# Kernel optimization log

Measured on AMD Instinct MI355X. Metric: run time of the kernel, lower is better.

The kernel has to match this reference:

```python
import jax, jax.numpy as jnp
import numpy as np

LN_EPS = 1e-5


def setup_inputs() -> dict:
    key = jax.random.key(0)
    ks = jax.random.split(key, 10)
    N, E, B = 20000, 320000, 16
    node_dim, cond_dim, out_dim = 256, 512, 256
    return {
        "node_feats": jax.random.normal(ks[0], (N, node_dim), dtype=jnp.float32),
        "cond_feats": jax.random.normal(ks[1], (B, cond_dim), dtype=jnp.float32),
        "batch_ids": jax.random.randint(ks[2], (N,), 0, B),
        "node_j_ids": jax.random.randint(ks[3], (E,), 0, N),
        "node_i_ids": jax.random.randint(ks[4], (E,), 0, N),
        "edge_w": jax.random.uniform(ks[5], (E, 1), dtype=jnp.float32),
        "edge_p": jax.random.uniform(ks[6], (E, 1), dtype=jnp.float32),
        "Wc": jax.random.normal(ks[7], (cond_dim, 2 * out_dim), dtype=jnp.float32) * (cond_dim ** -0.5),
        "bc": jax.random.normal(ks[8], (2 * out_dim,), dtype=jnp.float32) * 0.02,
        "Wl": jax.random.normal(ks[9], (node_dim, out_dim), dtype=jnp.float32) * (node_dim ** -0.5),
    }


def reference(node_feats, cond_feats, batch_ids, node_j_ids, node_i_ids,
              edge_w, edge_p, Wc, bc, Wl):
    N = node_feats.shape[0]
    # --- FiLM fusion ---
    gb = cond_feats @ Wc + bc                       # [B, 2*out_dim]
    gamma, beta = jnp.split(gb, 2, axis=-1)
    gamma = gamma + 1.0
    x = node_feats @ Wl                             # [N, out_dim]
    # non-affine LayerNorm over last dim
    mu = jnp.mean(x, axis=-1, keepdims=True)
    var = jnp.mean(jnp.square(x - mu), axis=-1, keepdims=True)
    x = (x - mu) * jax.lax.rsqrt(var + LN_EPS)
    x = x * gamma[batch_ids] + beta[batch_ids]      # per-node FiLM via batch gather
    x = jax.nn.relu(x)
    # --- message passing: gather -> weight -> scatter-add ---
    edge_weights = edge_w * edge_p                  # [E, 1]
    msg = x[node_j_ids] * edge_weights              # [E, out_dim]
    agg = jax.ops.segment_sum(msg, node_i_ids, num_segments=N)
    return jax.nn.relu(agg)
```

## Files before the change

### kernel.cpp

```cpp
#include <hip/hip_runtime.h>
#include <hip/hip_bf16.h>

#define OUT_DIM 256
#define COND_DIM 512
#define NODE_DIM 256
#define TM 32
#define LDA 264
#define LN_EPS 1e-5f
#define CAP 64
#define POISON 0xAAAAAAAAu
#define CHUNK 4096
#define EPT 16
#define NBINS 256
#define BCAP 2560

typedef __attribute__((ext_vector_type(8))) short bf16x8;
typedef __attribute__((ext_vector_type(8))) unsigned short u16x8;
typedef __attribute__((ext_vector_type(4))) float f32x4;

__device__ inline unsigned short f2bf(float f) {
    unsigned u = __float_as_uint(f);
    u += 0x7fffu + ((u >> 16) & 1u);
    return (unsigned short)(u >> 16);
}
__device__ inline float bf2f(unsigned short b) {
    return __uint_as_float((unsigned)b << 16);
}

__global__ __launch_bounds__(256) void f1_prep_kernel(
        const int* __restrict__ ni, const int* __restrict__ nj,
        const float* __restrict__ ew, const float* __restrict__ ep,
        unsigned* __restrict__ gcur, unsigned* __restrict__ coarse_ij,
        float* __restrict__ coarse_w, int E, int f1b,
        const float* __restrict__ Wl, unsigned short* __restrict__ WlT,
        const float* __restrict__ cond, const float* __restrict__ Wc,
        const float* __restrict__ bc, float* __restrict__ gamma, float* __restrict__ beta) {
    __shared__ float lds[64 * 65];
    __shared__ unsigned cnt[NBINS], base[NBINS];
    int t = threadIdx.x;

    if (blockIdx.x < (unsigned)f1b) {
        cnt[t] = 0;
        __syncthreads();
        unsigned ijr[EPT]; float wr[EPT]; unsigned rbr[EPT];
        int e0 = blockIdx.x * CHUNK;
        #pragma unroll
        for (int k = 0; k < EPT; ++k) {
            int e = e0 + k * 256 + t;
            if (e < E) {
                unsigned i = (unsigned)ni[e];
                unsigned j = (unsigned)nj[e];
                float w = ew[e] * ep[e];
                unsigned b = i >> 7;
                unsigned r = atomicAdd(&cnt[b], 1u);
                ijr[k] = (i << 16) | j;
                wr[k]  = w;
                rbr[k] = r | (b << 20);
            } else rbr[k] = 0xFFFFFFFFu;
        }
        __syncthreads();
        {
            unsigned c = cnt[t];
            base[t] = c ? (atomicAdd(&gcur[t], c) - POISON) : 0u;
        }
        __syncthreads();
        #pragma unroll
        for (int k = 0; k < EPT; ++k) {
            if (rbr[k] != 0xFFFFFFFFu) {
                unsigned b = rbr[k] >> 20;
                unsigned pos = base[b] + (rbr[k] & 0xFFFFFu);
                if (pos < BCAP) {
                    unsigned idx = b * BCAP + pos;
                    coarse_ij[idx] = ijr[k];
                    coarse_w[idx]  = wr[k];
                }
            }
        }
        return;
    }

    int pb = blockIdx.x - f1b;
    if (pb < 16) {
        float (*tile)[65] = (float(*)[65])lds;
        int bx = pb & 3, by = pb >> 2;
        int tr = t >> 6, tc = t & 63;
        #pragma unroll
        for (int rr = 0; rr < 64; rr += 4)
            tile[rr + tr][tc] = Wl[(by * 64 + rr + tr) * OUT_DIM + bx * 64 + tc];
        __syncthreads();
        #pragma unroll
        for (int rr = 0; rr < 64; rr += 4) {
            int n = bx * 64 + rr + tr;
            int k = by * 64 + tc;
            WlT[n * NODE_DIM + k] = f2bf(tile[tc][rr + tr]);
        }
    } else {
        int bf = pb - 16;
        int b = bf >> 1, half = bf & 1;
        int o = half * 256 + t;
        float* c = lds;
        for (int k = t; k < COND_DIM; k += 256) c[k] = cond[b * COND_DIM + k];
        __syncthreads();
        float acc = bc[o];
        for (int k = 0; k < COND_DIM; k += 4) {
            float4 cv = *(const float4*)&c[k];
            acc += cv.x * Wc[(k + 0) * 512 + o];
            acc += cv.y * Wc[(k + 1) * 512 + o];
            acc += cv.z * Wc[(k + 2) * 512 + o];
            acc += cv.w * Wc[(k + 3) * 512 + o];
        }
        if (half == 0) gamma[b * 256 + t] = acc + 1.0f;
        else           beta[b * 256 + t] = acc;
    }
}

__global__ __launch_bounds__(256) void f2_gemm_kernel(
        const unsigned* __restrict__ gcur, const unsigned* __restrict__ coarse_ij,
        const float* __restrict__ coarse_w, unsigned* __restrict__ epk,
        unsigned* __restrict__ cursor, int NB,
        const float* __restrict__ nf, const unsigned short* __restrict__ WlT,
        const int* __restrict__ batch_ids, const float* __restrict__ gamma,
        const float* __restrict__ beta, unsigned short* __restrict__ xout, int N) {
    __shared__ __align__(16) unsigned short Atile[TM * LDA];
    __shared__ float part_s[TM][2], part_s2[TM][2];
    __shared__ int bid_s[TM];
    __shared__ unsigned lcur[128];
    int t = threadIdx.x;

    if (blockIdx.x < (unsigned)NB) {
        int b = blockIdx.x;
        if (t < 128) lcur[t] = 0;
        __syncthreads();
        unsigned cntb = gcur[b] - POISON;
        if (cntb > BCAP) cntb = BCAP;
        for (unsigned r = t; r < cntb; r += 256) {
            unsigned ij = coarse_ij[(unsigned)b * BCAP + r];
            float w = coarse_w[(unsigned)b * BCAP + r];
            unsigned i = ij >> 16;
            unsigned c = atomicAdd(&lcur[i & 127u], 1u);
            if (c < CAP)
                epk[(i << 6) + c] = (ij & 0xFFFFu) | ((unsigned)f2bf(w) << 16);
        }
        __syncthreads();
        if (t < 128) cursor[(unsigned)b * 128 + t] = lcur[t];
        return;
    }

    int n0 = (blockIdx.x - NB) * TM;

    #pragma unroll
    for (int it = 0; it < 8; ++it) {
        int idx = t + it * 256;
        int r = idx >> 6;
        int c4 = idx & 63;
        int row = n0 + r;
        float4 v;
        if (row < N) v = *(const float4*)&nf[(size_t)row * NODE_DIM + c4 * 4];
        else         v = make_float4(0.f, 0.f, 0.f, 0.f);
        unsigned* dst = (unsigned*)&Atile[r * LDA + c4 * 4];
        dst[0] = (unsigned)f2bf(v.x) | ((unsigned)f2bf(v.y) << 16);
        dst[1] = (unsigned)f2bf(v.z) | ((unsigned)f2bf(v.w) << 16);
    }
    if (t < TM) bid_s[t] = (n0 + t < N) ? batch_ids[n0 + t] : 0;
    __syncthreads();

    int wave = t >> 6;
    int lane = t & 63;
    int l = lane & 15;
    int quad = lane >> 4;
    int rowbase = (wave & 1) * 16;
    int colbase = (wave >> 1) * 128;
    int half = wave >> 1;

    f32x4 acc[8];
    #pragma unroll
    for (int ct = 0; ct < 8; ++ct) acc[ct] = (f32x4){0.f, 0.f, 0.f, 0.f};

    const unsigned short* Abase = &Atile[(rowbase + l) * LDA + quad * 8];
    const unsigned short* Bbase = &WlT[(colbase + l) * NODE_DIM + quad * 8];

    #pragma unroll
    for (int ks = 0; ks < 8; ++ks) {
        bf16x8 a = *(const bf16x8*)(Abase + ks * 32);
        #pragma unroll
        for (int ct = 0; ct < 8; ++ct) {
            bf16x8 b = *(const bf16x8*)(Bbase + ct * 16 * NODE_DIM + ks * 32);
            acc[ct] = __builtin_amdgcn_mfma_f32_16x16x32_bf16(a, b, acc[ct], 0, 0, 0);
        }
    }

    #pragma unroll
    for (int reg = 0; reg < 4; ++reg) {
        float s = 0.f, s2 = 0.f;
        #pragma unroll
        for (int ct = 0; ct < 8; ++ct) {
            float v = acc[ct][reg];
            s += v; s2 += v * v;
        }
        #pragma unroll
        for (int off = 1; off <= 8; off <<= 1) {
            s += __shfl_xor(s, off);
            s2 += __shfl_xor(s2, off);
        }
        if (l == 0) {
            int r = rowbase + quad * 4 + reg;
            part_s[r][half] = s;
            part_s2[r][half] = s2;
        }
    }
    __syncthreads();

    #pragma unroll
    for (int reg = 0; reg < 4; ++reg) {
        int lrow = rowbase + quad * 4 + reg;
        float S = part_s[lrow][0] + part_s[lrow][1];
        float S2 = part_s2[lrow][0] + part_s2[lrow][1];
        float mu = S * (1.f / OUT_DIM);
        float var = S2 * (1.f / OUT_DIM) - mu * mu;
        float rs = rsqrtf(var + LN_EPS);
        int grow = n0 + lrow;
        int bid = bid_s[lrow];
        const float* gg = &gamma[bid * OUT_DIM];
        const float* gb = &beta[bid * OUT_DIM];
        if (grow < N) {
            unsigned short* orow = &xout[(size_t)grow * OUT_DIM];
            #pragma unroll
            for (int ct = 0; ct < 8; ++ct) {
                int col = colbase + ct * 16 + l;
                float v = (acc[ct][reg] - mu) * rs;
                v = v * gg[col] + gb[col];
                orow[col] = f2bf(fmaxf(v, 0.f));
            }
        }
    }
}

__global__ void agg_kernel(const unsigned short* __restrict__ x, const unsigned* __restrict__ epk,
                           const unsigned* __restrict__ cursor, float* __restrict__ out, int N) {
    int node = blockIdx.x * 4 + (threadIdx.x >> 6);
    int lane = threadIdx.x & 63;
    if (node >= N) return;
    int deg = (int)cursor[node];
    if (deg > CAP) deg = CAP;
    int s = node << 6;
    int e = s + deg;
    int half = lane >> 5;
    int li = lane & 31;

    float a[8];
    #pragma unroll
    for (int k = 0; k < 8; ++k) a[k] = 0.f;

    for (int p = s; p < e; p += 8) {
        int i0 = p + 0 + half, i1 = p + 2 + half, i2 = p + 4 + half, i3 = p + 6 + half;
        unsigned pk0 = epk[i0];
        unsigned pk1 = epk[i1];
        unsigned pk2 = epk[i2];
        unsigned pk3 = epk[i3];
        u16x8 v0 = *(const u16x8*)&x[(size_t)(pk0 & 0xFFFFu) * OUT_DIM + li * 8];
        u16x8 v1 = *(const u16x8*)&x[(size_t)(pk1 & 0xFFFFu) * OUT_DIM + li * 8];
        u16x8 v2 = *(const u16x8*)&x[(size_t)(pk2 & 0xFFFFu) * OUT_DIM + li * 8];
        u16x8 v3 = *(const u16x8*)&x[(size_t)(pk3 & 0xFFFFu) * OUT_DIM + li * 8];
        float w0 = (i0 < e) ? bf2f((unsigned short)(pk0 >> 16)) : 0.f;
        float w1 = (i1 < e) ? bf2f((unsigned short)(pk1 >> 16)) : 0.f;
        float w2 = (i2 < e) ? bf2f((unsigned short)(pk2 >> 16)) : 0.f;
        float w3 = (i3 < e) ? bf2f((unsigned short)(pk3 >> 16)) : 0.f;
        #pragma unroll
        for (int k = 0; k < 8; ++k) {
            a[k] += bf2f(v0[k]) * w0;
            a[k] += bf2f(v1[k]) * w1;
            a[k] += bf2f(v2[k]) * w2;
            a[k] += bf2f(v3[k]) * w3;
        }
    }

    #pragma unroll
    for (int k = 0; k < 8; ++k) a[k] += __shfl_xor(a[k], 32);

    f32x4 o;
    int kb = half * 4;
    o[0] = fmaxf(a[kb + 0], 0.f);
    o[1] = fmaxf(a[kb + 1], 0.f);
    o[2] = fmaxf(a[kb + 2], 0.f);
    o[3] = fmaxf(a[kb + 3], 0.f);
    __builtin_nontemporal_store(o, (f32x4*)&out[(size_t)node * OUT_DIM + li * 8 + kb]);
}

extern "C" void kernel_launch(void* const* d_in, const int* in_sizes, int n_in,
                              void* d_out, int out_size, void* d_ws, size_t ws_size,
                              hipStream_t stream) {
    const float* node_feats = (const float*)d_in[0];
    const float* cond_feats = (const float*)d_in[1];
    const int*   batch_ids  = (const int*)d_in[2];
    const int*   node_j     = (const int*)d_in[3];
    const int*   node_i     = (const int*)d_in[4];
    const float* edge_w     = (const float*)d_in[5];
    const float* edge_p     = (const float*)d_in[6];
    const float* Wc         = (const float*)d_in[7];
    const float* bc         = (const float*)d_in[8];
    const float* Wl         = (const float*)d_in[9];
    float* out = (float*)d_out;

    const int N = in_sizes[2];
    const int E = in_sizes[3];
    const int B = in_sizes[1] / COND_DIM;

    const int NB = (N + 127) / 128;

    char* ws = (char*)d_ws;
    float* gamma     = (float*)ws;  ws += (size_t)B * OUT_DIM * 4;
    float* beta      = (float*)ws;  ws += (size_t)B * OUT_DIM * 4;
    unsigned short* x   = (unsigned short*)ws;  ws += (size_t)N * OUT_DIM * 2;
    unsigned short* WlT = (unsigned short*)ws;  ws += (size_t)NODE_DIM * OUT_DIM * 2;
    unsigned* cursor = (unsigned*)ws;  ws += (size_t)NB * 128 * 4;
    unsigned* epk    = (unsigned*)ws;  ws += (size_t)N * CAP * 4;
    unsigned* gcur   = (unsigned*)ws;  ws += (size_t)NBINS * 4;
    unsigned* coarse_ij = (unsigned*)ws;  ws += (size_t)NBINS * BCAP * 4;
    float*    coarse_w  = (float*)ws;     ws += (size_t)NBINS * BCAP * 4;

    int nblk = (N + TM - 1) / TM;
    int f1b = (E + CHUNK - 1) / CHUNK;

    f1_prep_kernel<<<f1b + 48, 256, 0, stream>>>(node_j == node_j ? node_i : node_i, node_j,
                                                 edge_w, edge_p,
                                                 gcur, coarse_ij, coarse_w, E, f1b,
                                                 Wl, WlT, cond_feats, Wc, bc, gamma, beta);
    f2_gemm_kernel<<<NB + nblk, 256, 0, stream>>>(gcur, coarse_ij, coarse_w, epk, cursor, NB,
                                                  node_feats, WlT, batch_ids,
                                                  gamma, beta, x, N);
    agg_kernel<<<(N + 3) / 4, 256, 0, stream>>>(x, epk, cursor, out, N);
}
```

Baseline: 152.3 us.

## Quantize node features to per-row uint8 with scale for gather aggregation

The GEMM/LayerNorm/FiLM kernel now stores post-ReLU node features as 8-bit unsigned values with a per-row max-based scale instead of bf16. The aggregation kernel gathers 8 bytes per lane instead of 16 and folds the row scale into the edge weight, halving gather traffic on the bandwidth-bound message-passing step. This costs an extra reduction pass and a sync in the GEMM epilogue, and the 8-bit precision loss may breach accuracy tolerance.

```diff
diff --git a/kernel.cpp b/kernel.cpp
--- a/kernel.cpp
+++ b/kernel.cpp
@@ -15,7 +15,6 @@
 #define BCAP 2560
 
 typedef __attribute__((ext_vector_type(8))) short bf16x8;
-typedef __attribute__((ext_vector_type(8))) unsigned short u16x8;
 typedef __attribute__((ext_vector_type(4))) float f32x4;
 
 __device__ inline unsigned short f2bf(float f) {
@@ -120,9 +119,10 @@
         unsigned* __restrict__ cursor, int NB,
         const float* __restrict__ nf, const unsigned short* __restrict__ WlT,
         const int* __restrict__ batch_ids, const float* __restrict__ gamma,
-        const float* __restrict__ beta, unsigned short* __restrict__ xout, int N) {
+        const float* __restrict__ beta, unsigned char* __restrict__ xq,
+        float* __restrict__ xscale, int N) {
     __shared__ __align__(16) unsigned short Atile[TM * LDA];
-    __shared__ float part_s[TM][2], part_s2[TM][2];
+    __shared__ float part_s[TM][2], part_s2[TM][2], part_mx[TM][2];
     __shared__ int bid_s[TM];
     __shared__ unsigned lcur[128];
     int t = threadIdx.x;
@@ -210,6 +210,7 @@
     }
     __syncthreads();
 
+    float mu_r[4], rs_r[4];
     #pragma unroll
     for (int reg = 0; reg < 4; ++reg) {
         int lrow = rowbase + quad * 4 + reg;
@@ -217,25 +218,59 @@
         float S2 = part_s2[lrow][0] + part_s2[lrow][1];
         float mu = S * (1.f / OUT_DIM);
         float var = S2 * (1.f / OUT_DIM) - mu * mu;
-        float rs = rsqrtf(var + LN_EPS);
+        mu_r[reg] = mu;
+        rs_r[reg] = rsqrtf(var + LN_EPS);
+    }
+
+    #pragma unroll
+    for (int reg = 0; reg < 4; ++reg) {
+        int lrow = rowbase + quad * 4 + reg;
         int grow = n0 + lrow;
         int bid = bid_s[lrow];
         const float* gg = &gamma[bid * OUT_DIM];
         const float* gb = &beta[bid * OUT_DIM];
         if (grow < N) {
-            unsigned short* orow = &xout[(size_t)grow * OUT_DIM];
+            float mx = 0.f;
             #pragma unroll
             for (int ct = 0; ct < 8; ++ct) {
                 int col = colbase + ct * 16 + l;
-                float v = (acc[ct][reg] - mu) * rs;
-                v = v * gg[col] + gb[col];
-                orow[col] = f2bf(fmaxf(v, 0.f));
+                float v = (acc[ct][reg] - mu_r[reg]) * rs_r[reg];
+                v = fmaxf(v * gg[col] + gb[col], 0.f);
+                mx = fmaxf(mx, v);
             }
-        }
-    }
-}
-
-__global__ void agg_kernel(const unsigned short* __restrict__ x, const unsigned* __restrict__ epk,
+            #pragma unroll
+            for (int off = 1; off <= 8; off <<= 1)
+                mx = fmaxf(mx, __shfl_xor(mx, off));
+            if (l == 0) part_mx[lrow][half] = mx;
+        }
+    }
+    __syncthreads();
+
+    #pragma unroll
+    for (int reg = 0; reg < 4; ++reg) {
+        int lrow = rowbase + quad * 4 + reg;
+        int grow = n0 + lrow;
+        int bid = bid_s[lrow];
+        const float* gg = &gamma[bid * OUT_DIM];
+        const float* gb = &beta[bid * OUT_DIM];
+        if (grow < N) {
+            float mx = fmaxf(part_mx[lrow][0], part_mx[lrow][1]);
+            float inv = (mx > 0.f) ? 255.f / mx : 0.f;
+            if (half == 0 && l == 0) xscale[grow] = mx * (1.f / 255.f);
+            unsigned char* orow = &xq[(size_t)grow * OUT_DIM];
+            #pragma unroll
+            for (int ct = 0; ct < 8; ++ct) {
+                int col = colbase + ct * 16 + l;
+                float v = (acc[ct][reg] - mu_r[reg]) * rs_r[reg];
+                v = fmaxf(v * gg[col] + gb[col], 0.f);
+                orow[col] = (unsigned char)rintf(v * inv);
+            }
+        }
+    }
+}
+
+__global__ void agg_kernel(const unsigned char* __restrict__ xq, const float* __restrict__ xscale,
+                           const unsigned* __restrict__ epk,
                            const unsigned* __restrict__ cursor, float* __restrict__ out, int N) {
     int node = blockIdx.x * 4 + (threadIdx.x >> 6);
     int lane = threadIdx.x & 63;
@@ -257,21 +292,34 @@
         unsigned pk1 = epk[i1];
         unsigned pk2 = epk[i2];
         unsigned pk3 = epk[i3];
-        u16x8 v0 = *(const u16x8*)&x[(size_t)(pk0 & 0xFFFFu) * OUT_DIM + li * 8];
-        u16x8 v1 = *(const u16x8*)&x[(size_t)(pk1 & 0xFFFFu) * OUT_DIM + li * 8];
-        u16x8 v2 = *(const u16x8*)&x[(size_t)(pk2 & 0xFFFFu) * OUT_DIM + li * 8];
-        u16x8 v3 = *(const u16x8*)&x[(size_t)(pk3 & 0xFFFFu) * OUT_DIM + li * 8];
-        float w0 = (i0 < e) ? bf2f((unsigned short)(pk0 >> 16)) : 0.f;
-        float w1 = (i1 < e) ? bf2f((unsigned short)(pk1 >> 16)) : 0.f;
-        float w2 = (i2 < e) ? bf2f((unsigned short)(pk2 >> 16)) : 0.f;
-        float w3 = (i3 < e) ? bf2f((unsigned short)(pk3 >> 16)) : 0.f;
-        #pragma unroll
-        for (int k = 0; k < 8; ++k) {
-            a[k] += bf2f(v0[k]) * w0;
-            a[k] += bf2f(v1[k]) * w1;
-            a[k] += bf2f(v2[k]) * w2;
-            a[k] += bf2f(v3[k]) * w3;
-        }
+        uint2 q0 = *(const uint2*)&xq[(size_t)(pk0 & 0xFFFFu) * OUT_DIM + li * 8];
+        uint2 q1 = *(const uint2*)&xq[(size_t)(pk1 & 0xFFFFu) * OUT_DIM + li * 8];
+        uint2 q2 = *(const uint2*)&xq[(size_t)(pk2 & 0xFFFFu) * OUT_DIM + li * 8];
+        uint2 q3 = *(const uint2*)&xq[(size_t)(pk3 & 0xFFFFu) * OUT_DIM + li * 8];
+        float s0 = xscale[pk0 & 0xFFFFu];
+        float s1 = xscale[pk1 & 0xFFFFu];
+        float s2 = xscale[pk2 & 0xFFFFu];
+        float s3 = xscale[pk3 & 0xFFFFu];
+        float w0 = (i0 < e) ? bf2f((unsigned short)(pk0 >> 16)) * s0 : 0.f;
+        float w1 = (i1 < e) ? bf2f((unsigned short)(pk1 >> 16)) * s1 : 0.f;
+        float w2 = (i2 < e) ? bf2f((unsigned short)(pk2 >> 16)) * s2 : 0.f;
+        float w3 = (i3 < e) ? bf2f((unsigned short)(pk3 >> 16)) * s3 : 0.f;
+        a[0] += (float)(q0.x & 0xFFu) * w0;         a[0] += (float)(q1.x & 0xFFu) * w1;
+        a[1] += (float)((q0.x >> 8) & 0xFFu) * w0;  a[1] += (float)((q1.x >> 8) & 0xFFu) * w1;
+        a[2] += (float)((q0.x >> 16) & 0xFFu) * w0; a[2] += (float)((q1.x >> 16) & 0xFFu) * w1;
+        a[3] += (float)(q0.x >> 24) * w0;           a[3] += (float)(q1.x >> 24) * w1;
+        a[4] += (float)(q0.y & 0xFFu) * w0;         a[4] += (float)(q1.y & 0xFFu) * w1;
+        a[5] += (float)((q0.y >> 8) & 0xFFu) * w0;  a[5] += (float)((q1.y >> 8) & 0xFFu) * w1;
+        a[6] += (float)((q0.y >> 16) & 0xFFu) * w0; a[6] += (float)((q1.y >> 16) & 0xFFu) * w1;
+        a[7] += (float)(q0.y >> 24) * w0;           a[7] += (float)(q1.y >> 24) * w1;
+        a[0] += (float)(q2.x & 0xFFu) * w2;         a[0] += (float)(q3.x & 0xFFu) * w3;
+        a[1] += (float)((q2.x >> 8) & 0xFFu) * w2;  a[1] += (float)((q3.x >> 8) & 0xFFu) * w3;
+        a[2] += (float)((q2.x >> 16) & 0xFFu) * w2; a[2] += (float)((q3.x >> 16) & 0xFFu) * w3;
+        a[3] += (float)(q2.x >> 24) * w2;           a[3] += (float)(q3.x >> 24) * w3;
+        a[4] += (float)(q2.y & 0xFFu) * w2;         a[4] += (float)(q3.y & 0xFFu) * w3;
+        a[5] += (float)((q2.y >> 8) & 0xFFu) * w2;  a[5] += (float)((q3.y >> 8) & 0xFFu) * w3;
+        a[6] += (float)((q2.y >> 16) & 0xFFu) * w2; a[6] += (float)((q3.y >> 16) & 0xFFu) * w3;
+        a[7] += (float)(q2.y >> 24) * w2;           a[7] += (float)(q3.y >> 24) * w3;
     }
 
     #pragma unroll
@@ -310,7 +358,8 @@
     char* ws = (char*)d_ws;
     float* gamma     = (float*)ws;  ws += (size_t)B * OUT_DIM * 4;
     float* beta      = (float*)ws;  ws += (size_t)B * OUT_DIM * 4;
-    unsigned short* x   = (unsigned short*)ws;  ws += (size_t)N * OUT_DIM * 2;
+    unsigned char* xq = (unsigned char*)ws;  ws += (size_t)N * OUT_DIM;
+    float* xscale    = (float*)ws;  ws += (size_t)N * 4;
     unsigned short* WlT = (unsigned short*)ws;  ws += (size_t)NODE_DIM * OUT_DIM * 2;
     unsigned* cursor = (unsigned*)ws;  ws += (size_t)NB * 128 * 4;
     unsigned* epk    = (unsigned*)ws;  ws += (size_t)N * CAP * 4;
@@ -321,12 +370,11 @@
     int nblk = (N + TM - 1) / TM;
     int f1b = (E + CHUNK - 1) / CHUNK;
 
-    f1_prep_kernel<<<f1b + 48, 256, 0, stream>>>(node_j == node_j ? node_i : node_i, node_j,
-                                                 edge_w, edge_p,
+    f1_prep_kernel<<<f1b + 48, 256, 0, stream>>>(node_i, node_j, edge_w, edge_p,
                                                  gcur, coarse_ij, coarse_w, E, f1b,
                                                  Wl, WlT, cond_feats, Wc, bc, gamma, beta);
     f2_gemm_kernel<<<NB + nblk, 256, 0, stream>>>(gcur, coarse_ij, coarse_w, epk, cursor, NB,
                                                   node_feats, WlT, batch_ids,
-                                                  gamma, beta, x, N);
-    agg_kernel<<<(N + 3) / 4, 256, 0, stream>>>(x, epk, cursor, out, N);
-}
+                                                  gamma, beta, xq, xscale, N);
+    agg_kernel<<<(N + 3) / 4, 256, 0, stream>>>(xq, xscale, epk, cursor, out, N);
+}
```

New measurement: 152.3 us. About the same (-0.0%).
